# Optimization experiments

Measured on AMD Instinct MI355X. Metric: run time of the kernel, lower is better.

The kernel has to match this reference:

```python
import jax, jax.numpy as jnp
import numpy as np


def setup_inputs() -> dict:
    key = jax.random.key(0)
    ks = jax.random.split(key, 8)
    T, S, W, O = 50000, 168, 336, 48
    N = T - W - O + 1
    x = jax.random.uniform(ks[0], (T,), minval=0.5, maxval=1.5, dtype=jnp.float32)
    noise = jax.random.normal(ks[1], (N, W), dtype=jnp.float32) * 0.001  # Normal(0, std=0.001)
    level_sc = jax.random.uniform(ks[2], (), minval=-1.0, maxval=1.0, dtype=jnp.float32)
    seas_sc = jax.random.uniform(ks[3], (), minval=-1.0, maxval=1.0, dtype=jnp.float32)
    init_seas = jax.random.uniform(ks[4], (S,), minval=0.65, maxval=1.35, dtype=jnp.float32)
    W1 = jax.random.normal(ks[5], (W, W), dtype=jnp.float32) / np.float32(np.sqrt(W))
    b1 = jnp.zeros((W,), jnp.float32)
    W2 = jax.random.normal(ks[6], (W, O), dtype=jnp.float32) / np.float32(np.sqrt(W))
    b2 = jnp.zeros((O,), jnp.float32)
    return {"x": x, "noise": noise, "level_sc": level_sc, "seas_sc": seas_sc,
            "init_seas": init_seas, "W1": W1, "b1": b1, "W2": W2, "b2": b2,
            "window_size": W, "out_size": O, "lvp": 1}


def reference(x, noise, level_sc, seas_sc, init_seas, W1, b1, W2, b2,
              window_size, out_size, lvp):
    T = x.shape[0]
    a = jax.nn.sigmoid(level_sc)      # level smoothing coeff
    g = jax.nn.sigmoid(seas_sc)       # seasonal smoothing coeff
    s0 = jnp.exp(init_seas)           # [S] initial multiplicative seasonals
    # seasonals list in torch: seas[0..S-1]=s0, seas[S]=s0[0], seas[S+i]=w_i.
    # Ring buffer holds seas[i..i+S-1] at step i (starting i=1): [s0[1:], s0[0]].
    buf0 = jnp.concatenate([s0[1:], s0[:1]])
    level0 = x[0] / s0[0]

    def step(carry, xi):
        level, buf = carry
        seas_i = buf[0]
        new_level = a * xi / seas_i + (1.0 - a) * level
        new_w = g * xi / new_level + (1.0 - g) * seas_i
        new_buf = jnp.concatenate([buf[1:], new_w[None]])
        return (new_level, new_buf), (new_level, new_w, jnp.log(new_level / level))

    _, (lvls, ws, logdiffs) = jax.lax.scan(step, (level0, buf0), x[1:])
    levels = jnp.concatenate([level0[None], lvls])        # [T]
    seas_full = jnp.concatenate([s0, s0[:1], ws])         # [S+T]

    d = logdiffs[1:] - logdiffs[:-1]
    level_var_loss = jnp.mean(d * d) * lvp

    N = T - window_size - out_size + 1
    idx_in = jnp.arange(N)[:, None] + jnp.arange(window_size)[None, :]   # [N,W]
    idx_lab = jnp.arange(N)[:, None] + window_size + jnp.arange(out_size)[None, :]  # [N,O]
    lev = levels[jnp.arange(N) + window_size][:, None]    # [N,1]
    inp = jnp.log(x[idx_in] / (lev * seas_full[idx_in])) + noise   # noisy squashed inputs
    labels = jnp.log(x[idx_lab] / (lev * seas_full[idx_lab]))

    h = jnp.tanh(inp @ W1 + b1)        # tanh_no_lstm: Linear(336,336)+tanh
    out = h @ W2 + b2                  # linear_no_lstm: Linear(336,48)
    return out, labels, level_var_loss
```

## Files before the change

kernel.cpp:

```cpp
#include <hip/hip_runtime.h>
#include <hip/hip_bf16.h>

typedef __attribute__((ext_vector_type(8))) short  s16x8;
typedef __attribute__((ext_vector_type(4))) short  s16x4;
typedef __attribute__((ext_vector_type(4))) float  f32x4;

#define T_LEN 50000
#define S_LEN 168
#define W_IN  336
#define O_OUT 48
#define N_ROWS (T_LEN - W_IN - O_OUT + 1)
#define N_PAD  49664
#define NBLK   (N_PAD / 64)

__device__ inline short f2bf(float f) {
    union { float f; unsigned u; } v; v.f = f;
    unsigned u = v.u;
    unsigned r = u + 0x7fffu + ((u >> 16) & 1u);
    return (short)(r >> 16);
}

__device__ inline int bfpk(float lo, float hi) {
    float2 f2; f2.x = lo; f2.y = hi;
    __hip_bfloat162 h = __float22bfloat162_rn(f2);
    int r; __builtin_memcpy(&r, &h, 4);
    return r;
}

__device__ inline float readlane_f(float v, int l) {
    return __int_as_float(__builtin_amdgcn_readlane(__float_as_int(v), l));
}

__device__ inline float fast_tanh(float v) {
    float e = __expf(2.f * v);
    return 1.f - 2.f * __builtin_amdgcn_rcpf(e + 1.f);
}

__global__ void k_preconvert(const float* __restrict__ W1, const float* __restrict__ W2,
                             short* __restrict__ W1T, short* __restrict__ W2T,
                             float* __restrict__ S1) {
    int idx = blockIdx.x * 256 + threadIdx.x;
    const int n1 = 352 * 352;
    const int n2 = n1 + 48 * 360;
    if (idx < n1) {
        int j = idx / 352, k = idx % 352;
        W1T[idx] = (j < 336 && k < 336) ? f2bf(W1[k * 336 + j]) : (short)0;
    } else if (idx < n2) {
        int i2 = idx - n1;
        int o = i2 / 360, k = i2 % 360;
        W2T[i2] = (k < 336) ? f2bf(W2[k * 48 + o]) : (short)0;
    } else if (idx < n2 + 352) {
        int j = idx - n2;
        float s = 0.f;
        if (j < 336)
            for (int k = 0; k < 336; ++k) s += W1[k * 336 + j];
        S1[j] = s;
    }
}

#define DPP_FMA(q_, CTRL, W, RM) { \
    int t_ = __builtin_amdgcn_update_dpp(0, __float_as_int(q_), (CTRL), (RM), 0xf, true); \
    q_ = fmaf((W), __int_as_float(t_), q_); }

__global__ void k_scan(const float* __restrict__ x, const float* __restrict__ level_sc,
                       const float* __restrict__ seas_sc, const float* __restrict__ init_seas,
                       float* __restrict__ lw, float* __restrict__ seasinit) {
    __shared__ float ring[256];
    int lane = threadIdx.x;
    float a = 1.f / (1.f + expf(-level_sc[0]));
    float g = 1.f / (1.f + expf(-seas_sc[0]));
    float om = 1.f - a, omg = 1.f - g;

    for (int t = lane; t < 256; t += 64) {
        float s = 1.f;
        if (t <= S_LEN) { s = expf(init_seas[t < S_LEN ? t : 0]); seasinit[t] = s; }
        ring[t] = s;
    }
    float lpv = x[0] / expf(init_seas[0]);
    if (lane == 0) { lw[0] = lpv; lw[1] = 1.f; }
    __syncthreads();

    float om1 = om, om2v = om1 * om1, om4 = om2v * om2v, om8 = om4 * om4;
    float pl    = powf(om, (float)(lane + 1));
    float fpre  = powf(om, (float)((lane & 15) + 1));
    float fpre2 = powf(om, (float)((lane & 31) + 1));

#define SCAN(QOUT, XV, RSV) { \
    float q_ = a * (XV) * (RSV); \
    DPP_FMA(q_, 0x111, om1,  0xf); \
    DPP_FMA(q_, 0x112, om2v, 0xf); \
    DPP_FMA(q_, 0x114, om4,  0xf); \
    DPP_FMA(q_, 0x118, om8,  0xf); \
    DPP_FMA(q_, 0x142, fpre,  0xa); \
    DPP_FMA(q_, 0x143, fpre2, 0xc); \
    QOUT = q_; }

#define XLOAD(I) float xr##I = x[1 + 64 * I + lane];
    XLOAD(0) XLOAD(1) XLOAD(2) XLOAD(3) XLOAD(4) XLOAD(5) XLOAD(6) XLOAD(7)
    XLOAD(8) XLOAD(9) XLOAD(10) XLOAD(11) XLOAD(12) XLOAD(13) XLOAD(14) XLOAD(15)
#undef XLOAD

    float sA0 = ring[1 + lane];
    float Qcur; SCAN(Qcur, xr0, __builtin_amdgcn_rcpf(sA0));
    float sW = sA0;
    float ldsA = ring[65 + lane];
    float ldsB;
    int ib = 1;

#define BODY(R, RN, LIN, LOUT, CLAMP) { \
    float lvl = fmaf(pl, lpv, Qcur); \
    lpv = readlane_f(lvl, 63); \
    float w_ = fmaf(omg, sW, (g * xr##R) * __builtin_amdgcn_rcpf(lvl)); \
    float2 pk_; pk_.x = lvl; pk_.y = w_; \
    *(float2*)&lw[2 * (ib + lane)] = pk_; \
    ring[(ib + S_LEN + lane) & 255] = w_; \
    LOUT = ring[(ib + 128 + lane) & 255]; \
    float Qn_; SCAN(Qn_, xr##RN, __builtin_amdgcn_rcpf(LIN)); \
    int pidx = ib + 1024 + lane; \
    if (CLAMP) pidx = pidx > (T_LEN - 1) ? (T_LEN - 1) : pidx; \
    xr##R = x[pidx]; \
    Qcur = Qn_; sW = LIN; \
    ib += 64; }

    for (int kb = 0; kb < 47; ++kb) {
        BODY(0,1,  ldsA, ldsB, 0) BODY(1,2,  ldsB, ldsA, 0) BODY(2,3,  ldsA, ldsB, 0) BODY(3,4,  ldsB, ldsA, 0)
        BODY(4,5,  ldsA, ldsB, 0) BODY(5,6,  ldsB, ldsA, 0) BODY(6,7,  ldsA, ldsB, 0) BODY(7,8,  ldsB, ldsA, 0)
        BODY(8,9,  ldsA, ldsB, 0) BODY(9,10, ldsB, ldsA, 0) BODY(10,11,ldsA, ldsB, 0) BODY(11,12,ldsB, ldsA, 0)
        BODY(12,13,ldsA, ldsB, 0) BODY(13,14,ldsB, ldsA, 0) BODY(14,15,ldsA, ldsB, 0) BODY(15,0, ldsB, ldsA, 0)
    }
    BODY(0,1,  ldsA, ldsB, 0) BODY(1,2,  ldsB, ldsA, 0) BODY(2,3,  ldsA, ldsB, 0) BODY(3,4,  ldsB, ldsA, 0)
    BODY(4,5,  ldsA, ldsB, 0) BODY(5,6,  ldsB, ldsA, 0) BODY(6,7,  ldsA, ldsB, 0) BODY(7,8,  ldsB, ldsA, 0)
    BODY(8,9,  ldsA, ldsB, 0) BODY(9,10, ldsB, ldsA, 0) BODY(10,11,ldsA, ldsB, 0) BODY(11,12,ldsB, ldsA, 0)
    BODY(12,13,ldsA, ldsB, 0)
    BODY(13,14,ldsB, ldsA, 1) BODY(14,15,ldsA, ldsB, 1) BODY(15,0, ldsB, ldsA, 1)
    BODY(0,1,  ldsA, ldsB, 1) BODY(1,2,  ldsB, ldsA, 1) BODY(2,3,  ldsA, ldsB, 1) BODY(3,4,  ldsB, ldsA, 1)
    BODY(4,5,  ldsA, ldsB, 1) BODY(5,6,  ldsB, ldsA, 1) BODY(6,7,  ldsA, ldsB, 1) BODY(7,8,  ldsB, ldsA, 1)
    BODY(8,9,  ldsA, ldsB, 1) BODY(9,10, ldsB, ldsA, 1) BODY(10,11,ldsA, ldsB, 1) BODY(11,12,ldsB, ldsA, 1)
#undef BODY

    {
        float lvl = fmaf(pl, lpv, Qcur);
        lpv = readlane_f(lvl, 63);
        float w_ = fmaf(omg, sW, (g * xr12) * __builtin_amdgcn_rcpf(lvl));
        float2 pk_; pk_.x = lvl; pk_.y = w_;
        *(float2*)&lw[2 * (49921 + lane)] = pk_;
    }
    {
        float Qn_; SCAN(Qn_, xr13, __builtin_amdgcn_rcpf(ldsA));
        float lvl = fmaf(pl, lpv, Qn_);
        if (lane < 15) {
            float w_ = fmaf(omg, ldsA, (g * xr13) * __builtin_amdgcn_rcpf(lvl));
            float2 pk_; pk_.x = lvl; pk_.y = w_;
            *(float2*)&lw[2 * (49985 + lane)] = pk_;
        }
    }
#undef SCAN
}

__global__ void k_logs(const float* __restrict__ x, const float* __restrict__ lw,
                       const float* __restrict__ seasinit,
                       float* __restrict__ F, float* __restrict__ llev,
                       float* __restrict__ partials) {
    __shared__ float sm[258];
    __shared__ float red[256];
    int tid = threadIdx.x;
    int t = blockIdx.x * 256 + tid;
    float ll = 0.f;
    if (t < T_LEN) {
        float2 cur = *(const float2*)&lw[2 * t];
        int ps = t - S_LEN; if (ps < 0) ps = 0;
        float sv = (t <= S_LEN) ? seasinit[t] : lw[2 * ps + 1];
        F[t]  = __logf(x[t]) - __logf(sv);
        ll    = __logf(cur.x);
        llev[t] = ll;
    }
    sm[tid] = ll;
    if (tid < 2) {
        int te = blockIdx.x * 256 + 256 + tid;
        sm[256 + tid] = (te < T_LEN) ? __logf(lw[2 * te]) : 0.f;
    }
    __syncthreads();
    float s = 0.f;
    if (t < T_LEN - 2) {
        float d = sm[tid + 2] - 2.f * sm[tid + 1] + sm[tid];
        s = d * d;
    }
    red[tid] = s; __syncthreads();
    for (int off = 128; off > 0; off >>= 1) {
        if (tid < off) red[tid] += red[tid + off];
        __syncthreads();
    }
    if (tid == 0) partials[blockIdx.x] = red[0];
}

__global__ __launch_bounds__(512, 2) void k_gemm(
        const float* __restrict__ noise, const float* __restrict__ F,
        const float* __restrict__ llev, const short* __restrict__ W1T,
        const float* __restrict__ b1, const short* __restrict__ W2T,
        const float* __restrict__ b2, const float* __restrict__ S1,
        const float* __restrict__ partials, const int* __restrict__ lvp,
        float* __restrict__ out, float* __restrict__ labels, float* __restrict__ loss) {
    __shared__ __align__(16) short hlds[64][360];
    __shared__ __align__(16) float Flds[448];
    __shared__ __align__(16) float Llds[64];
    __shared__ __align__(16) float b1lds[352];
    __shared__ __align__(16) float S1lds[352];

    int t = threadIdx.x, w = t >> 6, l = t & 63;
    int lm = l & 15, lq = l >> 4;
    long n0 = (long)blockIdx.x * 64;

    if (blockIdx.x == 0 && w == 7) {
        float s = partials[l] + partials[l + 64] + partials[l + 128];
        if (l < 4) s += partials[l + 192];
#pragma unroll
        for (int off = 32; off > 0; off >>= 1) s += __shfl_down(s, off, 64);
        if (l == 0) loss[0] = s / (float)(T_LEN - 2) * (float)lvp[0];
    }

    if (t < 112)      *(f32x4*)&Flds[t * 4] = *(const f32x4*)&F[n0 + t * 4];
    else if (t < 128) *(f32x4*)&Llds[(t - 112) * 4] = *(const f32x4*)&llev[n0 + W_IN + (t - 112) * 4];
    else if (t < 216) {
        int i4 = (t - 128) * 4;
        f32x4 v = (f32x4){0.f, 0.f, 0.f, 0.f};
        if (i4 < W_IN) v = *(const f32x4*)&b1[i4];
        *(f32x4*)&b1lds[i4] = v;
    } else if (t < 304) {
        int i4 = (t - 216) * 4;
        *(f32x4*)&S1lds[i4] = *(const f32x4*)&S1[i4];
    }

    int rbase = (w >> 1) * 16;
    int jbase = (w & 1) * 176;
    long an0 = n0 + rbase + lm; if (an0 > N_ROWS - 2) an0 = N_ROWS - 2;
    const float* nr0 = noise + an0 * W_IN + lq * 8;

    f32x4 ncE0 = *(const f32x4*)&nr0[0],  ncE1 = *(const f32x4*)&nr0[4];
    f32x4 ncO0 = *(const f32x4*)&nr0[32], ncO1 = *(const f32x4*)&nr0[36];

    f32x4 acc[11];
#pragma unroll
    for (int c = 0; c < 11; ++c) acc[c] = (f32x4){0.f, 0.f, 0.f, 0.f};

    __syncthreads();

    const short* w1row = &W1T[(jbase + lm) * 352 + lq * 8];
#define LDW(CT, KS) (*(const s16x8*)&w1row[(CT) * 5632 + (KS) * 32])
#define MM(CT, AF) acc[CT] = __builtin_amdgcn_mfma_f32_16x16x32_bf16(AF, bf0, acc[CT], 0, 0, 0);

#define KSTEP(KS, NC0, NC1) { \
    s16x8 bf0; \
    { int fb = rbase + lm + (KS) * 32 + lq * 8; \
      int* b0i = (int*)&bf0; \
      b0i[0] = bfpk(Flds[fb+0] + NC0[0], Flds[fb+1] + NC0[1]); \
      b0i[1] = bfpk(Flds[fb+2] + NC0[2], Flds[fb+3] + NC0[3]); \
      b0i[2] = bfpk(Flds[fb+4] + NC1[0], Flds[fb+5] + NC1[1]); \
      b0i[3] = bfpk(Flds[fb+6] + NC1[2], Flds[fb+7] + NC1[3]); } \
    if ((KS) + 2 <= 10) { \
      NC0 = *(const f32x4*)&nr0[((KS)+2)*32]; \
      NC1 = *(const f32x4*)&nr0[((KS)+2)*32+4]; \
    } \
    s16x8 af0 = LDW(0,KS), af1 = LDW(1,KS), af2 = LDW(2,KS); \
    MM(0, af0)  af0 = LDW(3,KS); \
    MM(1, af1)  af1 = LDW(4,KS); \
    MM(2, af2)  af2 = LDW(5,KS); \
    MM(3, af0)  af0 = LDW(6,KS); \
    MM(4, af1)  af1 = LDW(7,KS); \
    MM(5, af2)  af2 = LDW(8,KS); \
    MM(6, af0)  af0 = LDW(9,KS); \
    MM(7, af1)  af1 = LDW(10,KS); \
    MM(8, af2) \
    MM(9, af0) \
    MM(10, af1) \
}

    KSTEP(0, ncE0, ncE1) KSTEP(1, ncO0, ncO1) KSTEP(2, ncE0, ncE1) KSTEP(3, ncO0, ncO1)
    KSTEP(4, ncE0, ncE1) KSTEP(5, ncO0, ncO1) KSTEP(6, ncE0, ncE1) KSTEP(7, ncO0, ncO1)
    KSTEP(8, ncE0, ncE1) KSTEP(9, ncO0, ncO1) KSTEP(10, ncE0, ncE1)
#undef KSTEP
#undef MM
#undef LDW

    float lv0 = Llds[rbase + lm];
#pragma unroll
    for (int ct = 0; ct < 11; ++ct) {
        f32x4 b1q = *(f32x4*)&b1lds[jbase + ct * 16 + lq * 4];
        f32x4 s1q = *(f32x4*)&S1lds[jbase + ct * 16 + lq * 4];
        int2 p0;
        p0.x = bfpk(fast_tanh(fmaf(-lv0, s1q[0], acc[ct][0] + b1q[0])),
                    fast_tanh(fmaf(-lv0, s1q[1], acc[ct][1] + b1q[1])));
        p0.y = bfpk(fast_tanh(fmaf(-lv0, s1q[2], acc[ct][2] + b1q[2])),
                    fast_tanh(fmaf(-lv0, s1q[3], acc[ct][3] + b1q[3])));
        *(int2*)&hlds[rbase + lm][jbase + ct * 16 + lq * 4] = p0;
    }
    __syncthreads();

    if (w < 4) {
        f32x4 a2[3];
        a2[0] = (f32x4){0,0,0,0}; a2[1] = (f32x4){0,0,0,0}; a2[2] = (f32x4){0,0,0,0};
#pragma unroll
        for (int ks = 0; ks < 11; ++ks) {
            s16x8 hf = *(s16x8*)&hlds[w * 16 + lm][ks * 32 + lq * 8];
#pragma unroll
            for (int ct = 0; ct < 3; ++ct) {
                s16x8 bf2 = *(const s16x8*)&W2T[(ct * 16 + lm) * 360 + ks * 32 + lq * 8];
                a2[ct] = __builtin_amdgcn_mfma_f32_16x16x32_bf16(hf, bf2, a2[ct], 0, 0, 0);
            }
        }
        int rloc = w * 16 + lq * 4;
#pragma unroll
        for (int ct = 0; ct < 3; ++ct) {
            float b2v = b2[ct * 16 + lm];
#pragma unroll
            for (int r = 0; r < 4; ++r) {
                long row = n0 + rloc + r;
                if (row < N_ROWS) out[row * O_OUT + ct * 16 + lm] = a2[ct][r] + b2v;
            }
        }
    } else {
        int rb2 = (w - 4) * 16;
        int lrow = l >> 2, cbase = (l & 3) * 12;
        long row = n0 + rb2 + lrow;
        if (row < N_ROWS) {
            float fl = -Llds[rb2 + lrow];
            const float* fp = &Flds[rb2 + lrow + W_IN + cbase];
            float* lp = &labels[row * O_OUT + cbase];
#pragma unroll
            for (int i = 0; i < 12; ++i) lp[i] = fp[i] + fl;
        }
    }
}

extern "C" void kernel_launch(void* const* d_in, const int* in_sizes, int n_in,
                              void* d_out, int out_size, void* d_ws, size_t ws_size,
                              hipStream_t stream) {
    const float* x         = (const float*)d_in[0];
    const float* noise     = (const float*)d_in[1];
    const float* level_sc  = (const float*)d_in[2];
    const float* seas_sc   = (const float*)d_in[3];
    const float* init_seas = (const float*)d_in[4];
    const float* W1        = (const float*)d_in[5];
    const float* b1        = (const float*)d_in[6];
    const float* W2        = (const float*)d_in[7];
    const float* b2        = (const float*)d_in[8];
    const int*   lvp       = (const int*)d_in[11];

    float* out    = (float*)d_out;
    float* labels = out + (long)N_ROWS * O_OUT;
    float* loss   = labels + (long)N_ROWS * O_OUT;

    float* wsf      = (float*)d_ws;
    float* lw       = wsf;
    float* seasinit = wsf + 100096;
    float* F        = wsf + 100288;
    float* llev     = wsf + 150464;
    float* partials = wsf + 200512;
    float* S1f      = wsf + 200768;
    short* W1T      = (short*)(wsf + 201152);
    short* W2T      = W1T + 352 * 352;

    k_preconvert<<<554, 256, 0, stream>>>(W1, W2, W1T, W2T, S1f);
    k_scan<<<1, 64, 0, stream>>>(x, level_sc, seas_sc, init_seas, lw, seasinit);
    k_logs<<<196, 256, 0, stream>>>(x, lw, seasinit, F, llev, partials);
    k_gemm<<<NBLK, 512, 0, stream>>>(noise, F, llev, W1T, b1, W2T, b2, S1f,
                                     partials, lvp, out, labels, loss);
}
```

Before: 175.2 us.

## Replace scan LDS ring with ds_bpermute and prefetch GEMM weights a k-step ahead

The sequential scan kernel no longer keeps the seasonal ring buffer in shared memory. It forwards the seasonal values needed 168 steps later through cross-lane ds_bpermute of the current and previous 64-wide blocks, which removes LDS store/load round trips from the serial dependency chain. The GEMM kernel now loads all 11 W1 fragments for the next k-step while the current MFMAs run, issues the first loads before the barrier, and raises the launch-bounds occupancy hint from 2 to 4. The extra live fragments raise register pressure while the higher occupancy hint tightens the register budget, which could cause spills.

```diff
diff --git a/kernel.cpp b/kernel.cpp
--- a/kernel.cpp
+++ b/kernel.cpp
@@ -65,25 +65,24 @@
 __global__ void k_scan(const float* __restrict__ x, const float* __restrict__ level_sc,
                        const float* __restrict__ seas_sc, const float* __restrict__ init_seas,
                        float* __restrict__ lw, float* __restrict__ seasinit) {
-    __shared__ float ring[256];
     int lane = threadIdx.x;
     float a = 1.f / (1.f + expf(-level_sc[0]));
     float g = 1.f / (1.f + expf(-seas_sc[0]));
     float om = 1.f - a, omg = 1.f - g;
 
-    for (int t = lane; t < 256; t += 64) {
-        float s = 1.f;
-        if (t <= S_LEN) { s = expf(init_seas[t < S_LEN ? t : 0]); seasinit[t] = s; }
-        ring[t] = s;
-    }
+    for (int t = lane; t <= S_LEN; t += 64)
+        seasinit[t] = expf(init_seas[t < S_LEN ? t : 0]);
+
     float lpv = x[0] / expf(init_seas[0]);
     if (lane == 0) { lw[0] = lpv; lw[1] = 1.f; }
-    __syncthreads();
 
     float om1 = om, om2v = om1 * om1, om4 = om2v * om2v, om8 = om4 * om4;
     float pl    = powf(om, (float)(lane + 1));
     float fpre  = powf(om, (float)((lane & 15) + 1));
     float fpre2 = powf(om, (float)((lane & 31) + 1));
+
+    int  idx4 = ((lane + 24) & 63) << 2;
+    bool lowj = (lane < 40);
 
 #define SCAN(QOUT, XV, RSV) { \
     float q_ = a * (XV) * (RSV); \
@@ -100,42 +99,43 @@
     XLOAD(8) XLOAD(9) XLOAD(10) XLOAD(11) XLOAD(12) XLOAD(13) XLOAD(14) XLOAD(15)
 #undef XLOAD
 
-    float sA0 = ring[1 + lane];
-    float Qcur; SCAN(Qcur, xr0, __builtin_amdgcn_rcpf(sA0));
-    float sW = sA0;
-    float ldsA = ring[65 + lane];
-    float ldsB;
+    float sW = expf(init_seas[1 + lane]);
+    float sN = expf(init_seas[65 + lane]);
+    int t105 = 105 + lane;
+    float wPrev = expf(init_seas[t105 >= S_LEN ? 0 : t105]);
+    float Qcur; SCAN(Qcur, xr0, __builtin_amdgcn_rcpf(sW));
     int ib = 1;
 
-#define BODY(R, RN, LIN, LOUT, CLAMP) { \
+#define BODY(R, RN, CLAMP) { \
     float lvl = fmaf(pl, lpv, Qcur); \
     lpv = readlane_f(lvl, 63); \
     float w_ = fmaf(omg, sW, (g * xr##R) * __builtin_amdgcn_rcpf(lvl)); \
     float2 pk_; pk_.x = lvl; pk_.y = w_; \
     *(float2*)&lw[2 * (ib + lane)] = pk_; \
-    ring[(ib + S_LEN + lane) & 255] = w_; \
-    LOUT = ring[(ib + 128 + lane) & 255]; \
-    float Qn_; SCAN(Qn_, xr##RN, __builtin_amdgcn_rcpf(LIN)); \
+    int tA_ = __builtin_amdgcn_ds_bpermute(idx4, __float_as_int(wPrev)); \
+    int tB_ = __builtin_amdgcn_ds_bpermute(idx4, __float_as_int(w_)); \
+    float sNN_ = lowj ? __int_as_float(tA_) : __int_as_float(tB_); \
+    float Qn_; SCAN(Qn_, xr##RN, __builtin_amdgcn_rcpf(sN)); \
     int pidx = ib + 1024 + lane; \
     if (CLAMP) pidx = pidx > (T_LEN - 1) ? (T_LEN - 1) : pidx; \
     xr##R = x[pidx]; \
-    Qcur = Qn_; sW = LIN; \
+    Qcur = Qn_; sW = sN; sN = sNN_; wPrev = w_; \
     ib += 64; }
 
     for (int kb = 0; kb < 47; ++kb) {
-        BODY(0,1,  ldsA, ldsB, 0) BODY(1,2,  ldsB, ldsA, 0) BODY(2,3,  ldsA, ldsB, 0) BODY(3,4,  ldsB, ldsA, 0)
-        BODY(4,5,  ldsA, ldsB, 0) BODY(5,6,  ldsB, ldsA, 0) BODY(6,7,  ldsA, ldsB, 0) BODY(7,8,  ldsB, ldsA, 0)
-        BODY(8,9,  ldsA, ldsB, 0) BODY(9,10, ldsB, ldsA, 0) BODY(10,11,ldsA, ldsB, 0) BODY(11,12,ldsB, ldsA, 0)
-        BODY(12,13,ldsA, ldsB, 0) BODY(13,14,ldsB, ldsA, 0) BODY(14,15,ldsA, ldsB, 0) BODY(15,0, ldsB, ldsA, 0)
-    }
-    BODY(0,1,  ldsA, ldsB, 0) BODY(1,2,  ldsB, ldsA, 0) BODY(2,3,  ldsA, ldsB, 0) BODY(3,4,  ldsB, ldsA, 0)
-    BODY(4,5,  ldsA, ldsB, 0) BODY(5,6,  ldsB, ldsA, 0) BODY(6,7,  ldsA, ldsB, 0) BODY(7,8,  ldsB, ldsA, 0)
-    BODY(8,9,  ldsA, ldsB, 0) BODY(9,10, ldsB, ldsA, 0) BODY(10,11,ldsA, ldsB, 0) BODY(11,12,ldsB, ldsA, 0)
-    BODY(12,13,ldsA, ldsB, 0)
-    BODY(13,14,ldsB, ldsA, 1) BODY(14,15,ldsA, ldsB, 1) BODY(15,0, ldsB, ldsA, 1)
-    BODY(0,1,  ldsA, ldsB, 1) BODY(1,2,  ldsB, ldsA, 1) BODY(2,3,  ldsA, ldsB, 1) BODY(3,4,  ldsB, ldsA, 1)
-    BODY(4,5,  ldsA, ldsB, 1) BODY(5,6,  ldsB, ldsA, 1) BODY(6,7,  ldsA, ldsB, 1) BODY(7,8,  ldsB, ldsA, 1)
-    BODY(8,9,  ldsA, ldsB, 1) BODY(9,10, ldsB, ldsA, 1) BODY(10,11,ldsA, ldsB, 1) BODY(11,12,ldsB, ldsA, 1)
+        BODY(0,1,0)  BODY(1,2,0)  BODY(2,3,0)  BODY(3,4,0)
+        BODY(4,5,0)  BODY(5,6,0)  BODY(6,7,0)  BODY(7,8,0)
+        BODY(8,9,0)  BODY(9,10,0) BODY(10,11,0) BODY(11,12,0)
+        BODY(12,13,0) BODY(13,14,0) BODY(14,15,0) BODY(15,0,0)
+    }
+    BODY(0,1,0)  BODY(1,2,0)  BODY(2,3,0)  BODY(3,4,0)
+    BODY(4,5,0)  BODY(5,6,0)  BODY(6,7,0)  BODY(7,8,0)
+    BODY(8,9,0)  BODY(9,10,0) BODY(10,11,0) BODY(11,12,0)
+    BODY(12,13,0)
+    BODY(13,14,1) BODY(14,15,1) BODY(15,0,1)
+    BODY(0,1,1)  BODY(1,2,1)  BODY(2,3,1)  BODY(3,4,1)
+    BODY(4,5,1)  BODY(5,6,1)  BODY(6,7,1)  BODY(7,8,1)
+    BODY(8,9,1)  BODY(9,10,1) BODY(10,11,1) BODY(11,12,1)
 #undef BODY
 
     {
@@ -146,10 +146,10 @@
         *(float2*)&lw[2 * (49921 + lane)] = pk_;
     }
     {
-        float Qn_; SCAN(Qn_, xr13, __builtin_amdgcn_rcpf(ldsA));
+        float Qn_; SCAN(Qn_, xr13, __builtin_amdgcn_rcpf(sN));
         float lvl = fmaf(pl, lpv, Qn_);
         if (lane < 15) {
-            float w_ = fmaf(omg, ldsA, (g * xr13) * __builtin_amdgcn_rcpf(lvl));
+            float w_ = fmaf(omg, sN, (g * xr13) * __builtin_amdgcn_rcpf(lvl));
             float2 pk_; pk_.x = lvl; pk_.y = w_;
             *(float2*)&lw[2 * (49985 + lane)] = pk_;
         }
@@ -193,7 +193,7 @@
     if (tid == 0) partials[blockIdx.x] = red[0];
 }
 
-__global__ __launch_bounds__(512, 2) void k_gemm(
+__global__ __launch_bounds__(512, 4) void k_gemm(
         const float* __restrict__ noise, const float* __restrict__ F,
         const float* __restrict__ llev, const short* __restrict__ W1T,
         const float* __restrict__ b1, const short* __restrict__ W2T,
@@ -235,48 +235,49 @@
     long an0 = n0 + rbase + lm; if (an0 > N_ROWS - 2) an0 = N_ROWS - 2;
     const float* nr0 = noise + an0 * W_IN + lq * 8;
 
-    f32x4 ncE0 = *(const f32x4*)&nr0[0],  ncE1 = *(const f32x4*)&nr0[4];
-    f32x4 ncO0 = *(const f32x4*)&nr0[32], ncO1 = *(const f32x4*)&nr0[36];
+    f32x4 nc0 = *(const f32x4*)&nr0[0], nc1 = *(const f32x4*)&nr0[4];
 
     f32x4 acc[11];
 #pragma unroll
     for (int c = 0; c < 11; ++c) acc[c] = (f32x4){0.f, 0.f, 0.f, 0.f};
-
-    __syncthreads();
 
     const short* w1row = &W1T[(jbase + lm) * 352 + lq * 8];
 #define LDW(CT, KS) (*(const s16x8*)&w1row[(CT) * 5632 + (KS) * 32])
+    s16x8 af0 = LDW(0,0), af1 = LDW(1,0), af2 = LDW(2,0), af3 = LDW(3,0), af4 = LDW(4,0),
+          af5 = LDW(5,0), af6 = LDW(6,0), af7 = LDW(7,0), af8 = LDW(8,0), af9 = LDW(9,0),
+          af10 = LDW(10,0);
+
+    __syncthreads();
+
 #define MM(CT, AF) acc[CT] = __builtin_amdgcn_mfma_f32_16x16x32_bf16(AF, bf0, acc[CT], 0, 0, 0);
 
-#define KSTEP(KS, NC0, NC1) { \
+#define KSTEP(KS) { \
     s16x8 bf0; \
     { int fb = rbase + lm + (KS) * 32 + lq * 8; \
       int* b0i = (int*)&bf0; \
-      b0i[0] = bfpk(Flds[fb+0] + NC0[0], Flds[fb+1] + NC0[1]); \
-      b0i[1] = bfpk(Flds[fb+2] + NC0[2], Flds[fb+3] + NC0[3]); \
-      b0i[2] = bfpk(Flds[fb+4] + NC1[0], Flds[fb+5] + NC1[1]); \
-      b0i[3] = bfpk(Flds[fb+6] + NC1[2], Flds[fb+7] + NC1[3]); } \
-    if ((KS) + 2 <= 10) { \
-      NC0 = *(const f32x4*)&nr0[((KS)+2)*32]; \
-      NC1 = *(const f32x4*)&nr0[((KS)+2)*32+4]; \
+      b0i[0] = bfpk(Flds[fb+0] + nc0[0], Flds[fb+1] + nc0[1]); \
+      b0i[1] = bfpk(Flds[fb+2] + nc0[2], Flds[fb+3] + nc0[3]); \
+      b0i[2] = bfpk(Flds[fb+4] + nc1[0], Flds[fb+5] + nc1[1]); \
+      b0i[3] = bfpk(Flds[fb+6] + nc1[2], Flds[fb+7] + nc1[3]); } \
+    if ((KS) < 10) { \
+      nc0 = *(const f32x4*)&nr0[((KS)+1)*32]; \
+      nc1 = *(const f32x4*)&nr0[((KS)+1)*32+4]; \
     } \
-    s16x8 af0 = LDW(0,KS), af1 = LDW(1,KS), af2 = LDW(2,KS); \
-    MM(0, af0)  af0 = LDW(3,KS); \
-    MM(1, af1)  af1 = LDW(4,KS); \
-    MM(2, af2)  af2 = LDW(5,KS); \
-    MM(3, af0)  af0 = LDW(6,KS); \
-    MM(4, af1)  af1 = LDW(7,KS); \
-    MM(5, af2)  af2 = LDW(8,KS); \
-    MM(6, af0)  af0 = LDW(9,KS); \
-    MM(7, af1)  af1 = LDW(10,KS); \
-    MM(8, af2) \
-    MM(9, af0) \
-    MM(10, af1) \
-}
-
-    KSTEP(0, ncE0, ncE1) KSTEP(1, ncO0, ncO1) KSTEP(2, ncE0, ncE1) KSTEP(3, ncO0, ncO1)
-    KSTEP(4, ncE0, ncE1) KSTEP(5, ncO0, ncO1) KSTEP(6, ncE0, ncE1) KSTEP(7, ncO0, ncO1)
-    KSTEP(8, ncE0, ncE1) KSTEP(9, ncO0, ncO1) KSTEP(10, ncE0, ncE1)
+    MM(0, af0)   if ((KS) < 10) af0  = LDW(0,  (KS)+1); \
+    MM(1, af1)   if ((KS) < 10) af1  = LDW(1,  (KS)+1); \
+    MM(2, af2)   if ((KS) < 10) af2  = LDW(2,  (KS)+1); \
+    MM(3, af3)   if ((KS) < 10) af3  = LDW(3,  (KS)+1); \
+    MM(4, af4)   if ((KS) < 10) af4  = LDW(4,  (KS)+1); \
+    MM(5, af5)   if ((KS) < 10) af5  = LDW(5,  (KS)+1); \
+    MM(6, af6)   if ((KS) < 10) af6  = LDW(6,  (KS)+1); \
+    MM(7, af7)   if ((KS) < 10) af7  = LDW(7,  (KS)+1); \
+    MM(8, af8)   if ((KS) < 10) af8  = LDW(8,  (KS)+1); \
+    MM(9, af9)   if ((KS) < 10) af9  = LDW(9,  (KS)+1); \
+    MM(10, af10) if ((KS) < 10) af10 = LDW(10, (KS)+1); \
+}
+
+    KSTEP(0) KSTEP(1) KSTEP(2) KSTEP(3) KSTEP(4) KSTEP(5)
+    KSTEP(6) KSTEP(7) KSTEP(8) KSTEP(9) KSTEP(10)
 #undef KSTEP
 #undef MM
 #undef LDW
```

After: 162.0 us. 7.5% less time.
